# Kernel optimization log

Measured on AMD Instinct MI355X. Metric: run time of the kernel, lower is better.

## Reference

```python
import jax, jax.numpy as jnp
import numpy as np

D_MODEL = 1024
EXPAND = 2
INNER = D_MODEL * EXPAND  # 2048
D_STATE = 64
K = 3
BSZ = 2
SEQ = 4096


def setup_inputs() -> dict:
    key = jax.random.key(0)
    ks = jax.random.split(key, 12)
    s = 0.02

    def w(k, shape):
        return jax.random.normal(k, shape, jnp.float32) * s

    return {
        "x": jax.random.normal(ks[0], (BSZ, SEQ, D_MODEL), jnp.float32),
        "W_in": w(ks[1], (D_MODEL, 2 * INNER)),
        "b_in": jnp.zeros((2 * INNER,), jnp.float32),
        "conv_w": w(ks[2], (INNER, K)),            # depthwise kernel per channel
        "conv_b": jnp.zeros((INNER,), jnp.float32),
        "W_dt": w(ks[3], (INNER, D_STATE)),
        "b_dt": jnp.zeros((D_STATE,), jnp.float32),
        "W_B": w(ks[4], (INNER, D_STATE)),
        "b_B": jnp.zeros((D_STATE,), jnp.float32),
        "W_C": w(ks[5], (INNER, D_STATE)),
        "b_C": jnp.zeros((D_STATE,), jnp.float32),
        "W_si": w(ks[6], (D_STATE, INNER)),
        "b_si": jnp.zeros((INNER,), jnp.float32),
        "D": jnp.ones((INNER,), jnp.float32),
        "W_out": w(ks[7], (INNER, D_MODEL)),
        "b_out": jnp.zeros((D_MODEL,), jnp.float32),
    }


def reference(x, W_in, b_in, conv_w, conv_b, W_dt, b_dt, W_B, b_B, W_C, b_C,
              W_si, b_si, D, W_out, b_out):
    bsz, seq_len, _ = x.shape
    inner = W_in.shape[1] // 2
    k = conv_w.shape[1]

    xz = x @ W_in + b_in                      # [B, L, 2*inner]
    x_main, gate = xz[..., :inner], xz[..., inner:]

    # Causal depthwise conv: torch pads k-1 both sides then slices [:L],
    # equivalent to left-pad (k-1), right-pad 0.
    lhs = jnp.transpose(x_main, (0, 2, 1))    # [B, C, L]
    rhs = conv_w[:, None, :]                  # [C, 1, K]
    conv = jax.lax.conv_general_dilated(
        lhs, rhs, window_strides=(1,), padding=[(k - 1, 0)],
        dimension_numbers=("NCH", "OIH", "NCH"), feature_group_count=inner)
    x_main = jnp.transpose(conv, (0, 2, 1)) + conv_b  # [B, L, inner]
    x_main = jax.nn.silu(x_main)

    dt = jax.nn.sigmoid(x_main @ W_dt + b_dt)  # [B, L, d_state]
    Bm = x_main @ W_B + b_B
    Cm = x_main @ W_C + b_C

    # Selective state recurrence: state_t = (1-dt_t)*state_{t-1} + dt_t*B_t
    def step(state, inp):
        dt_t, B_t, C_t = inp                  # each [B, d_state]
        state = (1.0 - dt_t) * state + dt_t * B_t
        return state, C_t * state

    xs = (jnp.moveaxis(dt, 1, 0), jnp.moveaxis(Bm, 1, 0), jnp.moveaxis(Cm, 1, 0))
    state0 = jnp.zeros((bsz, dt.shape[-1]), x.dtype)
    _, y = jax.lax.scan(step, state0, xs)     # [L, B, d_state]
    y = jnp.moveaxis(y, 0, 1)                 # [B, L, d_state]

    # LayerNorm over last dim, no affine, eps=1e-5 (torch F.layer_norm default)
    mu = jnp.mean(y, axis=-1, keepdims=True)
    var = jnp.var(y, axis=-1, keepdims=True)
    y = (y - mu) * jax.lax.rsqrt(var + 1e-5)

    y = y @ W_si + b_si                       # [B, L, inner]
    y = y + D * x_main
    y = y * jax.nn.sigmoid(gate)
    return y @ W_out + b_out                  # [B, L, d_model]
```

## Files before the change

### kernel.cpp

```cpp
#include <hip/hip_runtime.h>
#include <hip/hip_bf16.h>
#include <math.h>


namespace {

typedef __bf16 bf16x8 __attribute__((ext_vector_type(8)));
typedef float  f32x4  __attribute__((ext_vector_type(4)));
typedef unsigned short u16;

constexpr int kSeq = 4096;

__device__ __forceinline__ float sigmoid_f(float x) { return 1.0f / (1.0f + expf(-x)); }
__device__ __forceinline__ u16   f2bf(float f) { __bf16 h = (__bf16)f; return __builtin_bit_cast(u16, h); }
__device__ __forceinline__ float bf2f(u16 u)   { return (float)__builtin_bit_cast(__bf16, u); }

__device__ __forceinline__ void gll16(const u16* g, u16* l) {
    __builtin_amdgcn_global_load_lds(
        (const __attribute__((address_space(1))) unsigned int*)g,
        (__attribute__((address_space(3))) unsigned int*)l,
        16, 0, 0);
}

__device__ __forceinline__ int xcd_swizzle(int lin, int nwg) {
    const int q = nwg >> 3, r = nwg & 7;
    const int xcd = lin & 7, idx = lin >> 3;
    return (xcd < r ? xcd * (q + 1) : r * (q + 1) + (xcd - r) * q) + idx;
}

__device__ __forceinline__ void tr_body(float (*tile)[33],
                                        const float* __restrict__ in, u16* __restrict__ out,
                                        int R, int C, int r0, int c0, int t)
{
    const int lr = t >> 3, lc = (t & 7) * 4;
    float4 v = *reinterpret_cast<const float4*>(in + (size_t)(r0 + lr) * C + c0 + lc);
    tile[lr][lc + 0] = v.x; tile[lr][lc + 1] = v.y;
    tile[lr][lc + 2] = v.z; tile[lr][lc + 3] = v.w;
    __syncthreads();
    const int oc = t >> 3, orr = (t & 7) * 4;
    ushort4 o = make_ushort4(f2bf(tile[orr + 0][oc]), f2bf(tile[orr + 1][oc]),
                             f2bf(tile[orr + 2][oc]), f2bf(tile[orr + 3][oc]));
    *reinterpret_cast<ushort4*>(out + (size_t)(c0 + oc) * R + r0 + orr) = o;
}

__global__ __launch_bounds__(256)
void prep_all(const float* __restrict__ x,    u16* __restrict__ xb,
              const float* __restrict__ Win,  u16* __restrict__ WinT,
              const float* __restrict__ Wout, u16* __restrict__ WoutT,
              const float* __restrict__ Wdt,  const float* __restrict__ WB,
              const float* __restrict__ WC,   u16* __restrict__ WdtbcT,
              const float* __restrict__ Wsi,  u16* __restrict__ WsiT)
{
    const int t = threadIdx.x;
    int b = blockIdx.x;
    if (b < 8192) {
        long i = (long)b * 256 + t;
        float4 v = reinterpret_cast<const float4*>(x)[i];
        ushort4 o = make_ushort4(f2bf(v.x), f2bf(v.y), f2bf(v.z), f2bf(v.w));
        reinterpret_cast<ushort4*>(xb)[i] = o;
        return;
    }
    __shared__ float tile[32][33];
    b -= 8192;
    if (b < 4096) {
        tr_body(tile, Win, WinT, 1024, 4096, (b / 128) * 32, (b % 128) * 32, t);
        return;
    }
    b -= 4096;
    if (b < 2048) {
        tr_body(tile, Wout, WoutT, 2048, 1024, (b % 64) * 32, (b / 64) * 32, t);
        return;
    }
    b -= 2048;
    if (b < 384) {
        const int z = b / 128, rem = b % 128;
        const float* in = (z == 0) ? Wdt : (z == 1) ? WB : WC;
        u16* outp = WdtbcT + (size_t)z * 64 * 2048;
        tr_body(tile, in, outp, 2048, 64, (rem / 2) * 32, (rem % 2) * 32, t);
        return;
    }
    b -= 384;
    tr_body(tile, Wsi, WsiT, 64, 2048, (b % 2) * 32, (b / 2) * 32, t);
}

template <int BM, int BN, int BK, int WM, int WN, int MINW, int EPI>
__global__ __launch_bounds__(WM * WN * 64, MINW)
void gemm_mfma(const u16* __restrict__ A, const u16* __restrict__ Bt,
               const float* __restrict__ b0, const float* __restrict__ b1,
               const float* __restrict__ b2,
               const u16* __restrict__ aux0, const u16* __restrict__ aux1,
               void* __restrict__ o0, int N, int K, int nbx)
{
    constexpr int WAVES = WM * WN;
    constexpr int FM = BM / WM / 16, FN = BN / WN / 16;
    constexpr int LPR = BK / 8;
    constexpr int RPC = 64 / LPR;
    constexpr int CA  = BM * BK / 512 / WAVES;
    constexpr int CB  = BN * BK / 512 / WAVES;
    constexpr int NKK = BK / 32;
    __shared__ __align__(16) u16 As[BM][BK];
    __shared__ __align__(16) u16 Bs[BN][BK];

    const int tid  = threadIdx.x;
    const int lane = tid & 63;
    const int wid  = tid >> 6;
    const int wr   = (wid / WN) * (BM / WM);
    const int wc   = (wid % WN) * (BN / WN);
    const int swz  = xcd_swizzle(blockIdx.x, gridDim.x);
    const int row0 = (swz / nbx) * BM;
    const int col0 = (swz % nbx) * BN;

    const int srow = lane / LPR;
    const int slot = lane % LPR;
    const int fr   = lane & 15;
    const int fq   = lane >> 4;

    f32x4 acc[FM][FN];
#pragma unroll
    for (int m = 0; m < FM; ++m)
#pragma unroll
        for (int n = 0; n < FN; ++n) acc[m][n] = (f32x4){0.f, 0.f, 0.f, 0.f};

    for (int k0 = 0; k0 < K; k0 += BK) {
#pragma unroll
        for (int i = 0; i < CA; ++i) {
            const int c   = wid * CA + i;
            const int row = c * RPC + srow;
            const int sc  = (slot ^ (row & 7)) * 8;
            gll16(A + (size_t)(row0 + row) * K + k0 + sc,
                  &As[0][0] + c * 512 + lane * 8);
        }
#pragma unroll
        for (int i = 0; i < CB; ++i) {
            const int c   = wid * CB + i;
            const int row = c * RPC + srow;
            const int sc  = (slot ^ (row & 7)) * 8;
            gll16(Bt + (size_t)(col0 + row) * K + k0 + sc,
                  &Bs[0][0] + c * 512 + lane * 8);
        }
        __syncthreads();
#pragma unroll
        for (int kk = 0; kk < NKK; ++kk) {
            bf16x8 af[FM], bg[FN];
#pragma unroll
            for (int m = 0; m < FM; ++m) {
                const int rr = wr + m * 16 + fr;
                af[m] = *reinterpret_cast<const bf16x8*>(
                    &As[rr][((kk * 4 + fq) ^ (rr & 7)) * 8]);
            }
#pragma unroll
            for (int n = 0; n < FN; ++n) {
                const int rr = wc + n * 16 + fr;
                bg[n] = *reinterpret_cast<const bf16x8*>(
                    &Bs[rr][((kk * 4 + fq) ^ (rr & 7)) * 8]);
            }
#pragma unroll
            for (int m = 0; m < FM; ++m)
#pragma unroll
                for (int n = 0; n < FN; ++n)
                    acc[m][n] = __builtin_amdgcn_mfma_f32_16x16x32_bf16(af[m], bg[n], acc[m][n], 0, 0, 0);
        }
        __syncthreads();
    }

#pragma unroll
    for (int m = 0; m < FM; ++m) {
#pragma unroll
        for (int n = 0; n < FN; ++n) {
            const int gc  = col0 + wc + n * 16 + fr;
            const int gr0 = row0 + wr + m * 16 + fq * 4;
            if constexpr (EPI == 2) {
                float4 vv;
                float* vp = (float*)&vv;
#pragma unroll
                for (int j = 0; j < 4; ++j) {
                    float bb = (gc < 64) ? b0[gc] : (gc < 128) ? b1[gc - 64] : b2[gc - 128];
                    float v = acc[m][n][j] + bb;
                    if (gc < 64) v = sigmoid_f(v);
                    vp[j] = v;
                }
                *reinterpret_cast<float4*>(&((float*)o0)[(size_t)gc * 8192 + gr0]) = vv;
            } else {
#pragma unroll
                for (int j = 0; j < 4; ++j) {
                    const int gr = gr0 + j;
                    float v = acc[m][n][j];
                    if constexpr (EPI == 0) {
                        ((float*)o0)[(size_t)gr * N + gc] = v + b0[gc];
                    } else if constexpr (EPI == 1) {
                        ((u16*)o0)[(size_t)gr * N + gc] = f2bf(v + b0[gc]);
                    } else {
                        const size_t p = (size_t)gr * 2048 + gc;
                        float g  = bf2f(aux0[(size_t)gr * 4096 + gc]);
                        float xa = bf2f(aux1[p]);
                        v = v + b0[gc] + b1[gc] * xa;
                        ((u16*)o0)[p] = f2bf(v * sigmoid_f(g));
                    }
                }
            }
        }
    }
    (void)b1; (void)b2; (void)aux0; (void)aux1;
}

__global__ __launch_bounds__(256)
void conv_silu(const u16* __restrict__ xz, const float* __restrict__ cw,
               const float* __restrict__ cb, u16* __restrict__ xact)
{
    const size_t g  = ((size_t)blockIdx.x * 256 + threadIdx.x) * 8;
    const int    c0 = (int)(g & 2047);
    const size_t r  = g >> 11;
    const int    s  = (int)(r & (kSeq - 1));
    const u16* p = xz + r * 4096 + c0;
    u16 X0[8], X1[8] = {}, X2[8] = {};
    *reinterpret_cast<uint4*>(X0) = *reinterpret_cast<const uint4*>(p);
    if (s >= 1) *reinterpret_cast<uint4*>(X1) = *reinterpret_cast<const uint4*>(p - 4096);
    if (s >= 2) *reinterpret_cast<uint4*>(X2) = *reinterpret_cast<const uint4*>(p - 8192);
    u16 O[8];
#pragma unroll
    for (int j = 0; j < 8; ++j) {
        const int c = c0 + j;
        float v = bf2f(X2[j]) * cw[c * 3 + 0] + bf2f(X1[j]) * cw[c * 3 + 1]
                + bf2f(X0[j]) * cw[c * 3 + 2] + cb[c];
        O[j] = f2bf(v * sigmoid_f(v));
    }
    *reinterpret_cast<uint4*>(xact + r * 2048 + c0) = *reinterpret_cast<uint4*>(O);
}

__global__ __launch_bounds__(256)
void scan_kernel(const float* __restrict__ dtbcT, float* __restrict__ y)
{
    const int b = blockIdx.x >> 6;
    const int d = blockIdx.x & 63;
    const int t = threadIdx.x;
    const size_t col = (size_t)b * kSeq + t * 16;
    const float* dtp = dtbcT + (size_t)d         * 8192 + col;
    const float* Bp  = dtbcT + (size_t)(64 + d)  * 8192 + col;
    const float* Cp  = dtbcT + (size_t)(128 + d) * 8192 + col;

    float av[16], bv[16];
    float Acc = 1.f, Bcc = 0.f;
#pragma unroll
    for (int q = 0; q < 4; ++q) {
        float4 dv = *reinterpret_cast<const float4*>(dtp + q * 4);
        float4 Bv = *reinterpret_cast<const float4*>(Bp + q * 4);
        const float* dvp = (const float*)&dv;
        const float* bvp = (const float*)&Bv;
#pragma unroll
        for (int j = 0; j < 4; ++j) {
            const int i = q * 4 + j;
            float a  = 1.f - dvp[j];
            float bb = dvp[j] * bvp[j];
            av[i] = a; bv[i] = bb;
            Acc = a * Acc;
            Bcc = a * Bcc + bb;
        }
    }

    __shared__ float sA[256], sB[256];
    sA[t] = Acc; sB[t] = Bcc;
    __syncthreads();
    for (int off = 1; off < 256; off <<= 1) {
        float cA = sA[t], cB = sB[t];
        float pA = 1.f, pB = 0.f;
        if (t >= off) { pA = sA[t - off]; pB = sB[t - off]; }
        __syncthreads();
        if (t >= off) { sA[t] = cA * pA; sB[t] = cA * pB + cB; }
        __syncthreads();
    }

    float s = (t == 0) ? 0.f : sB[t - 1];
#pragma unroll
    for (int q = 0; q < 4; ++q) {
        float4 Cv = *reinterpret_cast<const float4*>(Cp + q * 4);
        const float* cvp = (const float*)&Cv;
#pragma unroll
        for (int j = 0; j < 4; ++j) {
            const int i = q * 4 + j;
            s = av[i] * s + bv[i];
            y[(col + i) * 64 + d] = cvp[j] * s;
        }
    }
}

__global__ __launch_bounds__(256)
void ln_kernel(const float* __restrict__ y, u16* __restrict__ ynb)
{
    const int w = threadIdx.x >> 6;
    const int l = threadIdx.x & 63;
    const size_t r = (size_t)blockIdx.x * 4 + w;
    float v  = y[r * 64 + l];
    float s  = v, s2 = v * v;
#pragma unroll
    for (int m = 1; m < 64; m <<= 1) {
        s  += __shfl_xor(s, m, 64);
        s2 += __shfl_xor(s2, m, 64);
    }
    float mu  = s * (1.f / 64.f);
    float var = s2 * (1.f / 64.f) - mu * mu;
    ynb[r * 64 + l] = f2bf((v - mu) * rsqrtf(var + 1e-5f));
}

}

extern "C" void kernel_launch(void* const* d_in, const int* in_sizes, int n_in,
                              void* d_out, int out_size, void* d_ws, size_t ws_size,
                              hipStream_t stream)
{
    (void)in_sizes; (void)n_in; (void)out_size; (void)ws_size;
    const float* x     = (const float*)d_in[0];
    const float* W_in  = (const float*)d_in[1];
    const float* b_in  = (const float*)d_in[2];
    const float* cw    = (const float*)d_in[3];
    const float* cb    = (const float*)d_in[4];
    const float* W_dt  = (const float*)d_in[5];
    const float* b_dt  = (const float*)d_in[6];
    const float* W_B   = (const float*)d_in[7];
    const float* b_B   = (const float*)d_in[8];
    const float* W_C   = (const float*)d_in[9];
    const float* b_C   = (const float*)d_in[10];
    const float* W_si  = (const float*)d_in[11];
    const float* b_si  = (const float*)d_in[12];
    const float* Dv    = (const float*)d_in[13];
    const float* W_out = (const float*)d_in[14];
    const float* b_out = (const float*)d_in[15];
    float* out = (float*)d_out;

    char* ws = (char*)d_ws;
    u16*   xzb    = (u16*)  (ws);
    u16*   xb     = (u16*)  (ws + 67108864);
    u16*   xact   = (u16*)  (ws + 83886080);
    u16*   hb     = (u16*)  (ws + 117440512);
    float* dtbcT  = (float*)(ws + 150994944);
    float* ybuf   = (float*)(ws + 157286400);
    u16*   ynb    = (u16*)  (ws + 159383552);
    u16*   WinT   = (u16*)  (ws + 160432128);
    u16*   WoutT  = (u16*)  (ws + 168820736);
    u16*   WdtbcT = (u16*)  (ws + 173015040);
    u16*   WsiT   = (u16*)  (ws + 173801472);

    dim3 blk(256);
    dim3 blk512(512);

    prep_all<<<dim3(8192 + 4096 + 2048 + 384 + 128), blk, 0, stream>>>(
        x, xb, W_in, WinT, W_out, WoutT, W_dt, W_B, W_C, WdtbcT, W_si, WsiT);

    gemm_mfma<128, 128, 64, 2, 4, 4, 1><<<dim3(32 * 64), blk512, 0, stream>>>(
        xb, WinT, b_in, nullptr, nullptr, nullptr, nullptr, xzb, 4096, 1024, 32);
    conv_silu<<<dim3(8192L * 2048 / (8 * 256)), blk, 0, stream>>>(xzb, cw, cb, xact);
    gemm_mfma<64, 64, 64, 2, 4, 4, 2><<<dim3(3 * 128), blk512, 0, stream>>>(
        xact, WdtbcT, b_dt, b_B, b_C, nullptr, nullptr, dtbcT, 192, 2048, 3);
    scan_kernel<<<dim3(128), blk, 0, stream>>>(dtbcT, ybuf);
    ln_kernel<<<dim3(8192 / 4), blk, 0, stream>>>(ybuf, ynb);
    gemm_mfma<128, 128, 64, 2, 4, 4, 3><<<dim3(16 * 64), blk512, 0, stream>>>(
        ynb, WsiT, b_si, Dv, nullptr, xzb + 2048, xact, hb, 2048, 64, 16);
    gemm_mfma<128, 128, 128, 2, 4, 4, 0><<<dim3(8 * 64), blk512, 0, stream>>>(
        hb, WoutT, b_out, nullptr, nullptr, nullptr, nullptr, out, 1024, 2048, 8);
}
```

Baseline: 232.1 us.

## Store scan output transposed and transpose through LDS in layernorm

The scan kernel now writes its output in a [d_state][row] transposed layout with contiguous float4 stores, replacing the strided scalar stores at 64-float stride. The layernorm kernel is rewritten to load 64x128 tiles of the transposed buffer into shared memory, reduce each row across the two halves of the block, and write bf16 rows. This removes uncoalesced writes from the scan, at the cost of an LDS transpose with a partial reduction and only 64 blocks for layernorm.

```diff
diff --git a/kernel.cpp b/kernel.cpp
--- a/kernel.cpp
+++ b/kernel.cpp
@@ -228,7 +228,7 @@
 }
 
 __global__ __launch_bounds__(256)
-void scan_kernel(const float* __restrict__ dtbcT, float* __restrict__ y)
+void scan_kernel(const float* __restrict__ dtbcT, float* __restrict__ yT)
 {
     const int b = blockIdx.x >> 6;
     const int d = blockIdx.x & 63;
@@ -274,31 +274,54 @@
     for (int q = 0; q < 4; ++q) {
         float4 Cv = *reinterpret_cast<const float4*>(Cp + q * 4);
         const float* cvp = (const float*)&Cv;
+        float4 ov;
+        float* op = (float*)&ov;
 #pragma unroll
         for (int j = 0; j < 4; ++j) {
             const int i = q * 4 + j;
             s = av[i] * s + bv[i];
-            y[(col + i) * 64 + d] = cvp[j] * s;
-        }
+            op[j] = cvp[j] * s;
+        }
+        *reinterpret_cast<float4*>(&yT[(size_t)d * 8192 + col + q * 4]) = ov;
     }
 }
 
 __global__ __launch_bounds__(256)
-void ln_kernel(const float* __restrict__ y, u16* __restrict__ ynb)
-{
-    const int w = threadIdx.x >> 6;
-    const int l = threadIdx.x & 63;
-    const size_t r = (size_t)blockIdx.x * 4 + w;
-    float v  = y[r * 64 + l];
-    float s  = v, s2 = v * v;
-#pragma unroll
-    for (int m = 1; m < 64; m <<= 1) {
-        s  += __shfl_xor(s, m, 64);
-        s2 += __shfl_xor(s2, m, 64);
-    }
-    float mu  = s * (1.f / 64.f);
-    float var = s2 * (1.f / 64.f) - mu * mu;
-    ynb[r * 64 + l] = f2bf((v - mu) * rsqrtf(var + 1e-5f));
+void ln_kernel(const float* __restrict__ yT, u16* __restrict__ ynb)
+{
+    __shared__ float tile[64][132];
+    __shared__ float ps[2][128], ps2[2][128];
+    const int t  = threadIdx.x;
+    const int r0 = blockIdx.x * 128;
+    const int d  = t >> 2;
+    const int cb = (t & 3) * 32;
+#pragma unroll
+    for (int j = 0; j < 8; ++j) {
+        float4 v = *reinterpret_cast<const float4*>(&yT[(size_t)d * 8192 + r0 + cb + j * 4]);
+        *reinterpret_cast<float4*>(&tile[d][cb + j * 4]) = v;
+    }
+    __syncthreads();
+    const int r = t & 127, h = t >> 7;
+    float s = 0.f, s2 = 0.f;
+#pragma unroll
+    for (int d2 = 0; d2 < 32; ++d2) {
+        float v = tile[h * 32 + d2][r];
+        s += v; s2 += v * v;
+    }
+    ps[h][r] = s; ps2[h][r] = s2;
+    __syncthreads();
+    const float S   = ps[0][r] + ps[1][r];
+    const float S2  = ps2[0][r] + ps2[1][r];
+    const float mu  = S * (1.f / 64.f);
+    const float inv = rsqrtf(S2 * (1.f / 64.f) - mu * mu + 1e-5f);
+    u16 o[32];
+#pragma unroll
+    for (int d2 = 0; d2 < 32; ++d2)
+        o[d2] = f2bf((tile[h * 32 + d2][r] - mu) * inv);
+#pragma unroll
+    for (int q = 0; q < 4; ++q)
+        *reinterpret_cast<uint4*>(&ynb[(size_t)(r0 + r) * 64 + h * 32 + q * 8]) =
+            *reinterpret_cast<const uint4*>(&o[q * 8]);
 }
 
 }
@@ -332,7 +355,7 @@
     u16*   xact   = (u16*)  (ws + 83886080);
     u16*   hb     = (u16*)  (ws + 117440512);
     float* dtbcT  = (float*)(ws + 150994944);
-    float* ybuf   = (float*)(ws + 157286400);
+    float* yT     = (float*)(ws + 157286400);
     u16*   ynb    = (u16*)  (ws + 159383552);
     u16*   WinT   = (u16*)  (ws + 160432128);
     u16*   WoutT  = (u16*)  (ws + 168820736);
@@ -350,8 +373,8 @@
     conv_silu<<<dim3(8192L * 2048 / (8 * 256)), blk, 0, stream>>>(xzb, cw, cb, xact);
     gemm_mfma<64, 64, 64, 2, 4, 4, 2><<<dim3(3 * 128), blk512, 0, stream>>>(
         xact, WdtbcT, b_dt, b_B, b_C, nullptr, nullptr, dtbcT, 192, 2048, 3);
-    scan_kernel<<<dim3(128), blk, 0, stream>>>(dtbcT, ybuf);
-    ln_kernel<<<dim3(8192 / 4), blk, 0, stream>>>(ybuf, ynb);
+    scan_kernel<<<dim3(128), blk, 0, stream>>>(dtbcT, yT);
+    ln_kernel<<<dim3(64), blk, 0, stream>>>(yT, ynb);
     gemm_mfma<128, 128, 64, 2, 4, 4, 3><<<dim3(16 * 64), blk512, 0, stream>>>(
         ynb, WsiT, b_si, Dv, nullptr, xzb + 2048, xact, hb, 2048, 64, 16);
     gemm_mfma<128, 128, 128, 2, 4, 4, 0><<<dim3(8 * 64), blk512, 0, stream>>>(
```

New measurement: 228.2 us. About the same (-1.7%).
